# Kernel optimization log

Hardware: AMD Instinct MI355X
Metric: run time of the kernel (lower is better)

The kernel has to match this reference:

```python
import jax, jax.numpy as jnp
import numpy as np

B, S, D = 4, 2048, 512
E, K = 8, 2
MH = 4 * D      # resmlp mlp hidden
EH = 2 * D      # expert hidden
EPS = 1e-5


def setup_inputs() -> dict:
    key = jax.random.key(0)
    ks = jax.random.split(key, 16)
    s = 0.02
    return {
        "x": jax.random.normal(ks[0], (B, S, D), dtype=jnp.float32),
        "ln1_g": jnp.ones((D,), jnp.float32), "ln1_b": jnp.zeros((D,), jnp.float32),
        "w1": jax.random.normal(ks[1], (D, MH), jnp.float32) * s,
        "b1": jnp.zeros((MH,), jnp.float32),
        "w2": jax.random.normal(ks[2], (MH, D), jnp.float32) * s,
        "b2": jnp.zeros((D,), jnp.float32),
        "ln2_g": jnp.ones((D,), jnp.float32), "ln2_b": jnp.zeros((D,), jnp.float32),
        "wr": jax.random.normal(ks[3], (E, D), jnp.float32) * s,
        "ew1": jax.random.normal(ks[4], (E, D, EH), jnp.float32) * s,
        "eb1": jnp.zeros((E, EH), jnp.float32),
        "ew2": jax.random.normal(ks[5], (E, EH, D), jnp.float32) * s,
        "eb2": jnp.zeros((E, D), jnp.float32),
        "lnf_g": jnp.ones((D,), jnp.float32), "lnf_b": jnp.zeros((D,), jnp.float32),
    }


def _ln(z, g, b):
    m = z.mean(-1, keepdims=True)
    v = ((z - m) ** 2).mean(-1, keepdims=True)
    return (z - m) * jax.lax.rsqrt(v + EPS) * g + b


def reference(x, ln1_g, ln1_b, w1, b1, w2, b2, ln2_g, ln2_b,
              wr, ew1, eb1, ew2, eb2, lnf_g, lnf_b):
    # ---- ResidualMLPBlock (eval mode: dropout is identity) ----
    h = _ln(x, ln1_g, ln1_b)
    h = jax.nn.gelu(h @ w1 + b1, approximate=False) @ w2 + b2
    x = x + h
    x = _ln(x, ln2_g, ln2_b) + x
    # ---- MoE (eval: no jitter noise, aux_loss = 0) ----
    xf = x.reshape(-1, D)              # [N, D], N = B*S
    n = xf.shape[0]
    probs = jax.nn.softmax(xf @ wr.T, axis=-1)          # [N, E]
    topv, topi = jax.lax.top_k(probs, K)                # [N, K]
    topv = topv / topv.sum(-1, keepdims=True)
    # dense per-token gate per expert: sum over k of renormalized prob where idx==j
    gates = jnp.zeros((n, E), xf.dtype).at[jnp.arange(n)[:, None], topi].add(topv)
    # per-expert MLP over all tokens (masked scatter-combine via gates)
    he = jax.nn.gelu(jnp.einsum("nd,edh->enh", xf, ew1) + eb1[:, None, :],
                     approximate=False)                 # [E, N, 2D]
    ye = jnp.einsum("enh,ehd->end", he, ew2) + eb2[:, None, :]  # [E, N, D]
    out = jnp.einsum("ne,end->nd", gates, ye).reshape(B, S, D)
    # ---- final LayerNorm ----
    out = _ln(out, lnf_g, lnf_b)
    aux_loss = jnp.zeros((), x.dtype)  # eval mode
    return out, aux_loss
```

## Files before the change

### kernel.cpp

```cpp
#include <hip/hip_runtime.h>

#define NTOK 8192
#define DIM  512
#define MHID 2048
#define EHID 1024
#define NEXP 8
#define RBLK 64

using half_t = _Float16;
typedef _Float16 f16x8 __attribute__((ext_vector_type(8)));
typedef float    f32x16 __attribute__((ext_vector_type(16)));

#define MFMA32(a, b, c) __builtin_amdgcn_mfma_f32_32x32x16_f16((a), (b), (c), 0, 0, 0)

typedef const __attribute__((address_space(1))) void* gas_ptr;
typedef __attribute__((address_space(3))) void*       las_ptr;
__device__ __forceinline__ void gl16(const void* g, void* l) {
    __builtin_amdgcn_global_load_lds((gas_ptr)g, (las_ptr)l, 16, 0, 0);
}

__device__ __forceinline__ float gelu_exact(float v) {
    return 0.5f * v * (1.0f + erff(v * 0.70710678118654752f));
}

__device__ __forceinline__ float block_sum4(float v, float* red, int tid) {
#pragma unroll
    for (int off = 32; off; off >>= 1) v += __shfl_down(v, off);
    if ((tid & 63) == 0) red[tid >> 6] = v;
    __syncthreads();
    float r = red[0] + red[1] + red[2] + red[3];
    __syncthreads();
    return r;
}

__global__ __launch_bounds__(256) void ln1_split_kernel(
    const float* __restrict__ x, const float* __restrict__ g, const float* __restrict__ b,
    half_t* __restrict__ xh, half_t* __restrict__ xl)
{
    const int row = blockIdx.x, tid = threadIdx.x;
    __shared__ float red[4];
    const size_t base = (size_t)row * DIM;
    float2 v = reinterpret_cast<const float2*>(x + base)[tid];
    float mean = block_sum4(v.x + v.y, red, tid) * (1.0f / DIM);
    float d0 = v.x - mean, d1 = v.y - mean;
    float var = block_sum4(d0 * d0 + d1 * d1, red, tid) * (1.0f / DIM);
    float rstd = rsqrtf(var + 1e-5f);
    int d = tid * 2;
    float y0 = d0 * rstd * g[d]     + b[d];
    float y1 = d1 * rstd * g[d + 1] + b[d + 1];
    half_t h0 = (half_t)y0, h1 = (half_t)y1;
    xh[base + d] = h0;  xh[base + d + 1] = h1;
    xl[base + d]     = (half_t)(y0 - (float)h0);
    xl[base + d + 1] = (half_t)(y1 - (float)h1);
}

__global__ __launch_bounds__(256) void resid_ln2_kernel(
    const float* __restrict__ x, float* __restrict__ p0, const float* __restrict__ p1,
    const float* __restrict__ b2,
    const float* __restrict__ g, const float* __restrict__ b,
    half_t* __restrict__ x3h)
{
    const int row = blockIdx.x, tid = threadIdx.x;
    __shared__ float red[4];
    const size_t base = (size_t)row * DIM;
    float2 xv = reinterpret_cast<const float2*>(x + base)[tid];
    float2 h0 = reinterpret_cast<float2*>(p0 + base)[tid];
    float2 h1 = reinterpret_cast<const float2*>(p1 + base)[tid];
    float2 bb = reinterpret_cast<const float2*>(b2)[tid];
    float z0 = xv.x + h0.x + h1.x + bb.x, z1 = xv.y + h0.y + h1.y + bb.y;
    float mean = block_sum4(z0 + z1, red, tid) * (1.0f / DIM);
    float d0 = z0 - mean, d1 = z1 - mean;
    float var = block_sum4(d0 * d0 + d1 * d1, red, tid) * (1.0f / DIM);
    float rstd = rsqrtf(var + 1e-5f);
    int d = tid * 2;
    float y0 = d0 * rstd * g[d]     + b[d]     + z0;
    float y1 = d1 * rstd * g[d + 1] + b[d + 1] + z1;
    float2 o; o.x = y0; o.y = y1;
    reinterpret_cast<float2*>(p0 + base)[tid] = o;
    x3h[base + d]     = (half_t)y0;
    x3h[base + d + 1] = (half_t)y1;
}

__global__ void transpose_split_kernel(const float* __restrict__ in,
                                       half_t* __restrict__ oh, half_t* __restrict__ ol,
                                       int R, int C)
{
    __shared__ float t[32][33];
    const size_t mo = (size_t)blockIdx.z * (size_t)R * (size_t)C;
    const int c0 = blockIdx.x * 32, r0 = blockIdx.y * 32;
    const int tx = threadIdx.x, ty = threadIdx.y;
    for (int i = ty; i < 32; i += 8) t[i][tx] = in[mo + (size_t)(r0 + i) * C + c0 + tx];
    __syncthreads();
    for (int i = ty; i < 32; i += 8) {
        float v = t[tx][i];
        size_t o = mo + (size_t)(c0 + i) * R + r0 + tx;
        half_t h = (half_t)v;
        oh[o] = h;
        if (ol) ol[o] = (half_t)(v - (float)h);
    }
}

template <int EPI>
__global__ __launch_bounds__(256) void gemm3_kernel(
    const half_t* __restrict__ A0, const half_t* __restrict__ A1,
    const half_t* __restrict__ B0, const half_t* __restrict__ B1,
    const float* __restrict__ bias,
    float* __restrict__ Cf0, float* __restrict__ Cf1,
    half_t* __restrict__ Ch, half_t* __restrict__ Cl,
    int Nc, int K, int Ktile)
{
    __shared__ __align__(16) half_t As0[2][128 * 32];
    __shared__ __align__(16) half_t As1[2][128 * 32];
    __shared__ __align__(16) half_t Bs0[2][128 * 32];
    __shared__ __align__(16) half_t Bs1[2][128 * 32];
    const int m0 = blockIdx.x * 128, n0 = blockIdx.y * 128;
    const int kbeg = blockIdx.z * Ktile;
    float* Cf = blockIdx.z ? Cf1 : Cf0;
    const int tid = threadIdx.x;
    const int lane = tid & 63, wid = tid >> 6;
    const int wr = wid >> 1, wc = wid & 1;

    const int c0 = tid, c1 = tid + 256;
    const int r0 = c0 >> 2, s0 = (c0 & 3) ^ ((r0 >> 1) & 3);
    const int r1 = c1 >> 2, s1 = (c1 & 3) ^ ((r1 >> 1) & 3);
    const size_t aoff0 = (size_t)(m0 + r0) * K + kbeg + s0 * 8;
    const size_t aoff1 = (size_t)(m0 + r1) * K + kbeg + s1 * 8;
    const size_t boff0 = (size_t)(n0 + r0) * K + kbeg + s0 * 8;
    const size_t boff1 = (size_t)(n0 + r1) * K + kbeg + s1 * 8;

    const int l31 = lane & 31, l5 = lane >> 5;
    int oa[2][2], ob[2][2];
#pragma unroll
    for (int i = 0; i < 2; i++)
#pragma unroll
        for (int kh = 0; kh < 2; kh++) {
            int ra = wr * 64 + i * 32 + l31;
            oa[i][kh] = ra * 32 + (((l5 + kh * 2) ^ ((ra >> 1) & 3)) << 3);
            int rb = wc * 64 + i * 32 + l31;
            ob[i][kh] = rb * 32 + (((l5 + kh * 2) ^ ((rb >> 1) & 3)) << 3);
        }

    f32x16 acc[2][2];
#pragma unroll
    for (int i = 0; i < 2; i++)
#pragma unroll
        for (int j = 0; j < 2; j++)
#pragma unroll
            for (int q = 0; q < 16; q++) acc[i][j][q] = 0.f;

    auto stage = [&](int bsel, int k0) {
        gl16(A0 + aoff0 + k0, &As0[bsel][c0 * 8]);
        gl16(A0 + aoff1 + k0, &As0[bsel][c1 * 8]);
        gl16(A1 + aoff0 + k0, &As1[bsel][c0 * 8]);
        gl16(A1 + aoff1 + k0, &As1[bsel][c1 * 8]);
        gl16(B0 + boff0 + k0, &Bs0[bsel][c0 * 8]);
        gl16(B0 + boff1 + k0, &Bs0[bsel][c1 * 8]);
        gl16(B1 + boff0 + k0, &Bs1[bsel][c0 * 8]);
        gl16(B1 + boff1 + k0, &Bs1[bsel][c1 * 8]);
    };
    auto compute = [&](int bsel) {
#pragma unroll
        for (int kh = 0; kh < 2; kh++) {
            f16x8 ah0 = *(const f16x8*)(&As0[bsel][0] + oa[0][kh]);
            f16x8 ah1 = *(const f16x8*)(&As0[bsel][0] + oa[1][kh]);
            f16x8 al0 = *(const f16x8*)(&As1[bsel][0] + oa[0][kh]);
            f16x8 al1 = *(const f16x8*)(&As1[bsel][0] + oa[1][kh]);
            f16x8 bh0 = *(const f16x8*)(&Bs0[bsel][0] + ob[0][kh]);
            f16x8 bh1 = *(const f16x8*)(&Bs0[bsel][0] + ob[1][kh]);
            f16x8 bl0 = *(const f16x8*)(&Bs1[bsel][0] + ob[0][kh]);
            f16x8 bl1 = *(const f16x8*)(&Bs1[bsel][0] + ob[1][kh]);
            acc[0][0] = MFMA32(ah0, bh0, acc[0][0]);
            acc[0][0] = MFMA32(al0, bh0, acc[0][0]);
            acc[0][0] = MFMA32(ah0, bl0, acc[0][0]);
            acc[0][1] = MFMA32(ah0, bh1, acc[0][1]);
            acc[0][1] = MFMA32(al0, bh1, acc[0][1]);
            acc[0][1] = MFMA32(ah0, bl1, acc[0][1]);
            acc[1][0] = MFMA32(ah1, bh0, acc[1][0]);
            acc[1][0] = MFMA32(al1, bh0, acc[1][0]);
            acc[1][0] = MFMA32(ah1, bl0, acc[1][0]);
            acc[1][1] = MFMA32(ah1, bh1, acc[1][1]);
            acc[1][1] = MFMA32(al1, bh1, acc[1][1]);
            acc[1][1] = MFMA32(ah1, bl1, acc[1][1]);
        }
    };

    stage(0, 0);
#pragma unroll 1
    for (int k0 = 0; k0 < Ktile; k0 += 64) {
        __syncthreads();
        if (k0 + 32 < Ktile) stage(1, k0 + 32);
        compute(0);
        __syncthreads();
        if (k0 + 64 < Ktile) stage(0, k0 + 64);
        compute(1);
    }

    const int er = 4 * l5;
#pragma unroll
    for (int i = 0; i < 2; i++)
#pragma unroll
        for (int j = 0; j < 2; j++) {
            int cc = n0 + wc * 64 + j * 32 + l31;
            float bv = (EPI == 1) ? bias[cc] : 0.f;
#pragma unroll
            for (int reg = 0; reg < 16; reg++) {
                int rr = m0 + wr * 64 + i * 32 + er + 8 * (reg >> 2) + (reg & 3);
                float v = acc[i][j][reg] + bv;
                size_t o = (size_t)rr * Nc + cc;
                if (EPI == 1) {
                    float ge = gelu_exact(v);
                    half_t h = (half_t)ge;
                    Ch[o] = h;
                    Cl[o] = (half_t)(ge - (float)h);
                } else {
                    Cf[o] = v;
                }
            }
        }
}

__global__ __launch_bounds__(256) void router_kernel(
    const float* __restrict__ x3, const float* __restrict__ wrm,
    int* __restrict__ cnt, int* __restrict__ aid, float* __restrict__ gate)
{
    __shared__ float wl[NEXP][DIM];
    __shared__ int   texp[RBLK * 2];
    __shared__ float tgate[RBLK * 2];
    __shared__ int   lslot[RBLK * 2];
    __shared__ int   lcnt[NEXP], lbase[NEXP];
    const int tid = threadIdx.x;
    for (int i = tid; i < NEXP * DIM / 4; i += 256)
        reinterpret_cast<float4*>(&wl[0][0])[i] = reinterpret_cast<const float4*>(wrm)[i];
    if (tid < NEXP) lcnt[tid] = 0;
    __syncthreads();
    const int w = tid >> 6, lane = tid & 63;
#pragma unroll 1
    for (int t = 0; t < RBLK / 4; ++t) {
        const int lt = w * (RBLK / 4) + t;
        const int token = blockIdx.x * RBLK + lt;
        const float* xr = x3 + (size_t)token * DIM;
        float a[NEXP];
#pragma unroll
        for (int e = 0; e < NEXP; e++) a[e] = 0.f;
#pragma unroll
        for (int d0 = 0; d0 < DIM; d0 += 64) {
            float xv = xr[d0 + lane];
#pragma unroll
            for (int e = 0; e < NEXP; e++) a[e] += xv * wl[e][d0 + lane];
        }
#pragma unroll
        for (int e = 0; e < NEXP; e++)
#pragma unroll
            for (int off = 32; off; off >>= 1) a[e] += __shfl_xor(a[e], off);
        if (lane == 0) {
            int i1 = 0; float v1 = a[0];
#pragma unroll
            for (int e = 1; e < NEXP; e++) if (a[e] > v1) { v1 = a[e]; i1 = e; }
            int i2 = -1; float v2 = -3.4e38f;
#pragma unroll
            for (int e = 0; e < NEXP; e++) if (e != i1 && a[e] > v2) { v2 = a[e]; i2 = e; }
            float e2 = expf(v2 - v1);
            float g1 = 1.0f / (1.0f + e2);
            texp[lt * 2]      = i1; tgate[lt * 2]      = g1;
            texp[lt * 2 + 1]  = i2; tgate[lt * 2 + 1]  = 1.0f - g1;
        }
    }
    __syncthreads();
    if (tid < RBLK * 2) lslot[tid] = atomicAdd(&lcnt[texp[tid]], 1);
    __syncthreads();
    if (tid < NEXP) lbase[tid] = atomicAdd(&cnt[tid * 32], lcnt[tid]);
    __syncthreads();
    if (tid < RBLK * 2) {
        const int e = texp[tid];
        const int asg = blockIdx.x * (RBLK * 2) + tid;
        aid[e * NTOK + lbase[e] + lslot[tid]] = asg;
        gate[asg] = tgate[tid];
    }
}

__global__ __launch_bounds__(256) void egemm1_kernel(
    const half_t* __restrict__ X,
    const half_t* __restrict__ W,
    const float* __restrict__ eb1,
    const int* __restrict__ cnt, const int* __restrict__ aid,
    half_t* __restrict__ He)
{
    const int bid = blockIdx.x;
    const int e = bid >> 9, rem = bid & 511;
    const int mt = rem >> 3, nt = rem & 7;
    const int ne = cnt[e * 32];
    if (mt * 128 >= ne) return;
    __shared__ __align__(16) half_t As[2][128 * 32];
    __shared__ __align__(16) half_t Bs[2][128 * 32];
    __shared__ int rowmap[128];
    const int tid = threadIdx.x;
    if (tid < 128) {
        int slot = mt * 128 + tid;
        rowmap[tid] = (slot < ne) ? aid[e * NTOK + slot] : -1;
    }
    __syncthreads();
    const int lane = tid & 63, wid = tid >> 6;
    const int wr = wid >> 1, wc = wid & 1;
    const int c0 = tid, c1 = tid + 256;
    const int r0 = c0 >> 2, s0 = (c0 & 3) ^ ((r0 >> 1) & 3);
    const int r1 = c1 >> 2, s1 = (c1 & 3) ^ ((r1 >> 1) & 3);
    const int a0r = rowmap[r0], a1r = rowmap[r1];
    const half_t* pa0 = X + (size_t)(a0r >= 0 ? (a0r >> 1) : 0) * DIM + s0 * 8;
    const half_t* pa1 = X + (size_t)(a1r >= 0 ? (a1r >> 1) : 0) * DIM + s1 * 8;
    const half_t* pb0 = W + (size_t)e * EHID * DIM + (size_t)(nt * 128 + r0) * DIM + s0 * 8;
    const half_t* pb1 = W + (size_t)e * EHID * DIM + (size_t)(nt * 128 + r1) * DIM + s1 * 8;

    const int l31 = lane & 31, l5 = lane >> 5;
    int oa[2][2], ob[2][2];
#pragma unroll
    for (int i = 0; i < 2; i++)
#pragma unroll
        for (int kh = 0; kh < 2; kh++) {
            int ra = wr * 64 + i * 32 + l31;
            oa[i][kh] = ra * 32 + (((l5 + kh * 2) ^ ((ra >> 1) & 3)) << 3);
            int rb = wc * 64 + i * 32 + l31;
            ob[i][kh] = rb * 32 + (((l5 + kh * 2) ^ ((rb >> 1) & 3)) << 3);
        }
    f32x16 acc[2][2];
#pragma unroll
    for (int i = 0; i < 2; i++)
#pragma unroll
        for (int j = 0; j < 2; j++)
#pragma unroll
            for (int q = 0; q < 16; q++) acc[i][j][q] = 0.f;

    auto stage = [&](int bsel, int k0) {
        gl16(pa0 + k0, &As[bsel][c0 * 8]);
        gl16(pa1 + k0, &As[bsel][c1 * 8]);
        gl16(pb0 + k0, &Bs[bsel][c0 * 8]);
        gl16(pb1 + k0, &Bs[bsel][c1 * 8]);
    };
    auto compute = [&](int bsel) {
#pragma unroll
        for (int kh = 0; kh < 2; kh++) {
            f16x8 a0 = *(const f16x8*)(&As[bsel][0] + oa[0][kh]);
            f16x8 a1 = *(const f16x8*)(&As[bsel][0] + oa[1][kh]);
            f16x8 b0 = *(const f16x8*)(&Bs[bsel][0] + ob[0][kh]);
            f16x8 b1 = *(const f16x8*)(&Bs[bsel][0] + ob[1][kh]);
            acc[0][0] = MFMA32(a0, b0, acc[0][0]);
            acc[0][1] = MFMA32(a0, b1, acc[0][1]);
            acc[1][0] = MFMA32(a1, b0, acc[1][0]);
            acc[1][1] = MFMA32(a1, b1, acc[1][1]);
        }
    };

    stage(0, 0);
#pragma unroll 1
    for (int k0 = 0; k0 < DIM; k0 += 64) {
        __syncthreads();
        if (k0 + 32 < DIM) stage(1, k0 + 32);
        compute(0);
        __syncthreads();
        if (k0 + 64 < DIM) stage(0, k0 + 64);
        compute(1);
    }
    const int er = 4 * l5;
#pragma unroll
    for (int i = 0; i < 2; i++)
#pragma unroll
        for (int reg = 0; reg < 16; reg++) {
            int rloc = wr * 64 + i * 32 + er + 8 * (reg >> 2) + (reg & 3);
            int a = rowmap[rloc];
            if (a >= 0) {
#pragma unroll
                for (int j = 0; j < 2; j++) {
                    int cc = nt * 128 + wc * 64 + j * 32 + l31;
                    float v = acc[i][j][reg] + eb1[e * EHID + cc];
                    He[(size_t)a * EHID + cc] = (half_t)gelu_exact(v);
                }
            }
        }
}

__global__ __launch_bounds__(256) void egemm2_kernel(
    const half_t* __restrict__ Hin,
    const half_t* __restrict__ W,
    const float* __restrict__ eb2,
    const int* __restrict__ cnt, const int* __restrict__ aid,
    const float* __restrict__ gate,
    float* __restrict__ Ye)
{
    const int bid = blockIdx.x;
    const int e = bid >> 8, rem = bid & 255;
    const int mt = rem >> 2, nt = rem & 3;
    const int ne = cnt[e * 32];
    if (mt * 128 >= ne) return;
    __shared__ __align__(16) half_t As[2][128 * 32];
    __shared__ __align__(16) half_t Bs[2][128 * 32];
    __shared__ int rowmap[128];
    const int tid = threadIdx.x;
    if (tid < 128) {
        int slot = mt * 128 + tid;
        rowmap[tid] = (slot < ne) ? aid[e * NTOK + slot] : -1;
    }
    __syncthreads();
    const int lane = tid & 63, wid = tid >> 6;
    const int wr = wid >> 1, wc = wid & 1;
    const int c0 = tid, c1 = tid + 256;
    const int r0 = c0 >> 2, s0 = (c0 & 3) ^ ((r0 >> 1) & 3);
    const int r1 = c1 >> 2, s1 = (c1 & 3) ^ ((r1 >> 1) & 3);
    const int a0r = rowmap[r0], a1r = rowmap[r1];
    const half_t* pa0 = Hin + (size_t)(a0r >= 0 ? a0r : 0) * EHID + s0 * 8;
    const half_t* pa1 = Hin + (size_t)(a1r >= 0 ? a1r : 0) * EHID + s1 * 8;
    const half_t* pb0 = W + (size_t)e * DIM * EHID + (size_t)(nt * 128 + r0) * EHID + s0 * 8;
    const half_t* pb1 = W + (size_t)e * DIM * EHID + (size_t)(nt * 128 + r1) * EHID + s1 * 8;

    const int l31 = lane & 31, l5 = lane >> 5;
    int oa[2][2], ob[2][2];
#pragma unroll
    for (int i = 0; i < 2; i++)
#pragma unroll
        for (int kh = 0; kh < 2; kh++) {
            int ra = wr * 64 + i * 32 + l31;
            oa[i][kh] = ra * 32 + (((l5 + kh * 2) ^ ((ra >> 1) & 3)) << 3);
            int rb = wc * 64 + i * 32 + l31;
            ob[i][kh] = rb * 32 + (((l5 + kh * 2) ^ ((rb >> 1) & 3)) << 3);
        }
    f32x16 acc[2][2];
#pragma unroll
    for (int i = 0; i < 2; i++)
#pragma unroll
        for (int j = 0; j < 2; j++)
#pragma unroll
            for (int q = 0; q < 16; q++) acc[i][j][q] = 0.f;

    auto stage = [&](int bsel, int k0) {
        gl16(pa0 + k0, &As[bsel][c0 * 8]);
        gl16(pa1 + k0, &As[bsel][c1 * 8]);
        gl16(pb0 + k0, &Bs[bsel][c0 * 8]);
        gl16(pb1 + k0, &Bs[bsel][c1 * 8]);
    };
    auto compute = [&](int bsel) {
#pragma unroll
        for (int kh = 0; kh < 2; kh++) {
            f16x8 a0 = *(const f16x8*)(&As[bsel][0] + oa[0][kh]);
            f16x8 a1 = *(const f16x8*)(&As[bsel][0] + oa[1][kh]);
            f16x8 b0 = *(const f16x8*)(&Bs[bsel][0] + ob[0][kh]);
            f16x8 b1 = *(const f16x8*)(&Bs[bsel][0] + ob[1][kh]);
            acc[0][0] = MFMA32(a0, b0, acc[0][0]);
            acc[0][1] = MFMA32(a0, b1, acc[0][1]);
            acc[1][0] = MFMA32(a1, b0, acc[1][0]);
            acc[1][1] = MFMA32(a1, b1, acc[1][1]);
        }
    };

    stage(0, 0);
#pragma unroll 1
    for (int k0 = 0; k0 < EHID; k0 += 64) {
        __syncthreads();
        if (k0 + 32 < EHID) stage(1, k0 + 32);
        compute(0);
        __syncthreads();
        if (k0 + 64 < EHID) stage(0, k0 + 64);
        compute(1);
    }
    const int er = 4 * l5;
#pragma unroll
    for (int i = 0; i < 2; i++)
#pragma unroll
        for (int reg = 0; reg < 16; reg++) {
            int rloc = wr * 64 + i * 32 + er + 8 * (reg >> 2) + (reg & 3);
            int a = rowmap[rloc];
            if (a >= 0) {
                float gv = gate[a];
#pragma unroll
                for (int j = 0; j < 2; j++) {
                    int cc = nt * 128 + wc * 64 + j * 32 + l31;
                    float v = (acc[i][j][reg] + eb2[e * DIM + cc]) * gv;
                    Ye[(size_t)a * DIM + cc] = v;
                }
            }
        }
}

__global__ __launch_bounds__(256) void combine_lnf_kernel(
    const float* __restrict__ Ye, const float* __restrict__ g, const float* __restrict__ b,
    float* __restrict__ out)
{
    const int t = blockIdx.x, tid = threadIdx.x;
    __shared__ float red[4];
    float2 y0 = reinterpret_cast<const float2*>(Ye + (size_t)(2 * t) * DIM)[tid];
    float2 y1 = reinterpret_cast<const float2*>(Ye + (size_t)(2 * t + 1) * DIM)[tid];
    float z0 = y0.x + y1.x, z1 = y0.y + y1.y;
    float mean = block_sum4(z0 + z1, red, tid) * (1.0f / DIM);
    float d0 = z0 - mean, d1 = z1 - mean;
    float var = block_sum4(d0 * d0 + d1 * d1, red, tid) * (1.0f / DIM);
    float rstd = rsqrtf(var + 1e-5f);
    int d = tid * 2;
    out[(size_t)t * DIM + d]     = d0 * rstd * g[d]     + b[d];
    out[(size_t)t * DIM + d + 1] = d1 * rstd * g[d + 1] + b[d + 1];
    if (t == 0 && tid == 0) out[(size_t)NTOK * DIM] = 0.f;
}

__global__ void zero_cnt_kernel(int* cnt) {
    cnt[threadIdx.x] = 0;
}

extern "C" void kernel_launch(void* const* d_in, const int* in_sizes, int n_in,
                              void* d_out, int out_size, void* d_ws, size_t ws_size,
                              hipStream_t stream)
{
    (void)in_sizes; (void)n_in; (void)out_size; (void)ws_size;
    const float* x    = (const float*)d_in[0];
    const float* ln1g = (const float*)d_in[1];
    const float* ln1b = (const float*)d_in[2];
    const float* w1   = (const float*)d_in[3];
    const float* b1   = (const float*)d_in[4];
    const float* w2   = (const float*)d_in[5];
    const float* b2   = (const float*)d_in[6];
    const float* ln2g = (const float*)d_in[7];
    const float* ln2b = (const float*)d_in[8];
    const float* wrm  = (const float*)d_in[9];
    const float* ew1  = (const float*)d_in[10];
    const float* eb1  = (const float*)d_in[11];
    const float* ew2  = (const float*)d_in[12];
    const float* eb2  = (const float*)d_in[13];
    const float* lnfg = (const float*)d_in[14];
    const float* lnfb = (const float*)d_in[15];
    float* out = (float*)d_out;

    char* w = (char*)d_ws;
    size_t off = 0;
    auto take = [&](size_t bytes) {
        char* p = w + off;
        off += bytes;
        off = (off + 255) & ~(size_t)255;
        return p;
    };
    half_t* xh_h  = (half_t*)take((size_t)NTOK * DIM * 2);
    half_t* xh_l  = (half_t*)take((size_t)NTOK * DIM * 2);
    half_t* w1t_h = (half_t*)take((size_t)DIM * MHID * 2);
    half_t* w1t_l = (half_t*)take((size_t)DIM * MHID * 2);
    half_t* w2t_h = (half_t*)take((size_t)MHID * DIM * 2);
    half_t* w2t_l = (half_t*)take((size_t)MHID * DIM * 2);
    char*   big   = take((size_t)NTOK * MHID * 2 * 2);
    half_t* a1h   = (half_t*)big;
    half_t* a1l   = (half_t*)(big + (size_t)NTOK * MHID * 2);
    half_t* heh   = (half_t*)big;
    float*  yef   = (float*)(big + (size_t)NTOK * MHID * 2);
    float*  x3f   = (float*)take((size_t)NTOK * DIM * 4);
    half_t* x3h   = (half_t*)take((size_t)NTOK * DIM * 2);
    half_t* ew1t  = (half_t*)take((size_t)NEXP * DIM * EHID * 2);
    half_t* ew2t  = (half_t*)take((size_t)NEXP * EHID * DIM * 2);
    int*    cnt   = (int*)take(1024);
    int*    aid   = (int*)take((size_t)NEXP * NTOK * 4);
    float*  gate  = (float*)take((size_t)NTOK * 2 * 4);

    float* p0 = x3f;
    float* p1 = (float*)xh_h;

    zero_cnt_kernel<<<1, 256, 0, stream>>>(cnt);
    ln1_split_kernel<<<NTOK, 256, 0, stream>>>(x, ln1g, ln1b, xh_h, xh_l);
    transpose_split_kernel<<<dim3(MHID / 32, DIM / 32, 1), dim3(32, 8), 0, stream>>>(w1, w1t_h, w1t_l, DIM, MHID);
    transpose_split_kernel<<<dim3(DIM / 32, MHID / 32, 1), dim3(32, 8), 0, stream>>>(w2, w2t_h, w2t_l, MHID, DIM);
    transpose_split_kernel<<<dim3(EHID / 32, DIM / 32, NEXP), dim3(32, 8), 0, stream>>>(ew1, ew1t, (half_t*)0, DIM, EHID);
    transpose_split_kernel<<<dim3(DIM / 32, EHID / 32, NEXP), dim3(32, 8), 0, stream>>>(ew2, ew2t, (half_t*)0, EHID, DIM);
    gemm3_kernel<1><<<dim3(NTOK / 128, MHID / 128, 1), 256, 0, stream>>>(
        xh_h, xh_l, w1t_h, w1t_l, b1, (float*)0, (float*)0, a1h, a1l, MHID, DIM, DIM);
    gemm3_kernel<0><<<dim3(NTOK / 128, DIM / 128, 2), 256, 0, stream>>>(
        a1h, a1l, w2t_h, w2t_l, (const float*)0, p0, p1, (half_t*)0, (half_t*)0, DIM, MHID, MHID / 2);
    resid_ln2_kernel<<<NTOK, 256, 0, stream>>>(x, p0, p1, b2, ln2g, ln2b, x3h);
    router_kernel<<<NTOK / RBLK, 256, 0, stream>>>(x3f, wrm, cnt, aid, gate);
    egemm1_kernel<<<NEXP * (NTOK / 128) * (EHID / 128), 256, 0, stream>>>(x3h, ew1t, eb1, cnt, aid, heh);
    egemm2_kernel<<<NEXP * (NTOK / 128) * (DIM / 128), 256, 0, stream>>>(heh, ew2t, eb2, cnt, aid, gate, yef);
    combine_lnf_kernel<<<NTOK, 256, 0, stream>>>(yef, lnfg, lnfb, out);
}
```

Before: 326.9 us.

## Enlarge residual-MLP split-precision GEMM tiles to 256-row, 8-wave blocks

Replaces the 128x128, 4-wave split-fp16 GEMM with a 512-thread kernel using 256x256 (first GEMM) or 256x128 (second GEMM) tiles. Each wave holds a 4xNREP grid of 32x32 accumulators, which raises operand reuse per LDS load. The pipeline now uses explicit vmcnt waits and raw s_barrier with one LDS buffer per k-step, and raises wave priority with s_setprio around the MFMA bursts. In exchange it uses more registers and LDS per block and launches fewer blocks, which may lower occupancy and load balance across CUs.

```diff
diff --git a/kernel.cpp b/kernel.cpp
--- a/kernel.cpp
+++ b/kernel.cpp
@@ -100,8 +100,8 @@
     }
 }
 
-template <int EPI>
-__global__ __launch_bounds__(256) void gemm3_kernel(
+template <int EPI, int NREP>
+__global__ __launch_bounds__(512, 2) void gemm8_kernel(
     const half_t* __restrict__ A0, const half_t* __restrict__ A1,
     const half_t* __restrict__ B0, const half_t* __restrict__ B1,
     const float* __restrict__ bias,
@@ -109,103 +109,122 @@
     half_t* __restrict__ Ch, half_t* __restrict__ Cl,
     int Nc, int K, int Ktile)
 {
-    __shared__ __align__(16) half_t As0[2][128 * 32];
-    __shared__ __align__(16) half_t As1[2][128 * 32];
-    __shared__ __align__(16) half_t Bs0[2][128 * 32];
-    __shared__ __align__(16) half_t Bs1[2][128 * 32];
-    const int m0 = blockIdx.x * 128, n0 = blockIdx.y * 128;
+    constexpr int BN    = NREP * 128;
+    constexpr int LOADS = 4 + 2 * NREP;
+    constexpr int TOT   = 16384 + NREP * 8192;
+    __shared__ __align__(16) half_t lds[2 * TOT];
+
+    const int m0 = blockIdx.x * 256, n0 = blockIdx.y * BN;
     const int kbeg = blockIdx.z * Ktile;
     float* Cf = blockIdx.z ? Cf1 : Cf0;
     const int tid = threadIdx.x;
     const int lane = tid & 63, wid = tid >> 6;
-    const int wr = wid >> 1, wc = wid & 1;
-
-    const int c0 = tid, c1 = tid + 256;
-    const int r0 = c0 >> 2, s0 = (c0 & 3) ^ ((r0 >> 1) & 3);
-    const int r1 = c1 >> 2, s1 = (c1 & 3) ^ ((r1 >> 1) & 3);
-    const size_t aoff0 = (size_t)(m0 + r0) * K + kbeg + s0 * 8;
-    const size_t aoff1 = (size_t)(m0 + r1) * K + kbeg + s1 * 8;
-    const size_t boff0 = (size_t)(n0 + r0) * K + kbeg + s0 * 8;
-    const size_t boff1 = (size_t)(n0 + r1) * K + kbeg + s1 * 8;
-
+    const int wr = wid >> 2, wc = wid & 3;
     const int l31 = lane & 31, l5 = lane >> 5;
-    int oa[2][2], ob[2][2];
-#pragma unroll
-    for (int i = 0; i < 2; i++)
+
+    const half_t* gsrc[LOADS];
+    {
+        const half_t* A0p = A0 + (size_t)m0 * K + kbeg;
+        const half_t* A1p = A1 + (size_t)m0 * K + kbeg;
+        const half_t* B0p = B0 + (size_t)n0 * K + kbeg;
+        const half_t* B1p = B1 + (size_t)n0 * K + kbeg;
+#pragma unroll
+        for (int i = 0; i < LOADS; i++) {
+            int c = tid + 512 * i;
+            const half_t* base; int cm;
+            if (c < 1024)                  { base = A0p; cm = c; }
+            else if (c < 2048)             { base = A1p; cm = c - 1024; }
+            else if (c < 2048 + NREP * 512){ base = B0p; cm = c - 2048; }
+            else                           { base = B1p; cm = c - 2048 - NREP * 512; }
+            int r = cm >> 2, ss = (cm & 3) ^ ((r >> 1) & 3);
+            gsrc[i] = base + (size_t)r * K + ss * 8;
+        }
+    }
+
+    int oa[4][2], ob[NREP][2];
+#pragma unroll
+    for (int m = 0; m < 4; m++)
 #pragma unroll
         for (int kh = 0; kh < 2; kh++) {
-            int ra = wr * 64 + i * 32 + l31;
-            oa[i][kh] = ra * 32 + (((l5 + kh * 2) ^ ((ra >> 1) & 3)) << 3);
-            int rb = wc * 64 + i * 32 + l31;
-            ob[i][kh] = rb * 32 + (((l5 + kh * 2) ^ ((rb >> 1) & 3)) << 3);
-        }
-
-    f32x16 acc[2][2];
-#pragma unroll
-    for (int i = 0; i < 2; i++)
-#pragma unroll
-        for (int j = 0; j < 2; j++)
-#pragma unroll
-            for (int q = 0; q < 16; q++) acc[i][j][q] = 0.f;
-
-    auto stage = [&](int bsel, int k0) {
-        gl16(A0 + aoff0 + k0, &As0[bsel][c0 * 8]);
-        gl16(A0 + aoff1 + k0, &As0[bsel][c1 * 8]);
-        gl16(A1 + aoff0 + k0, &As1[bsel][c0 * 8]);
-        gl16(A1 + aoff1 + k0, &As1[bsel][c1 * 8]);
-        gl16(B0 + boff0 + k0, &Bs0[bsel][c0 * 8]);
-        gl16(B0 + boff1 + k0, &Bs0[bsel][c1 * 8]);
-        gl16(B1 + boff0 + k0, &Bs1[bsel][c0 * 8]);
-        gl16(B1 + boff1 + k0, &Bs1[bsel][c1 * 8]);
-    };
-    auto compute = [&](int bsel) {
+            int ra = wr * 128 + m * 32 + l31;
+            oa[m][kh] = ra * 32 + (((l5 + 2 * kh) ^ ((ra >> 1) & 3)) << 3);
+        }
+#pragma unroll
+    for (int n = 0; n < NREP; n++)
 #pragma unroll
         for (int kh = 0; kh < 2; kh++) {
-            f16x8 ah0 = *(const f16x8*)(&As0[bsel][0] + oa[0][kh]);
-            f16x8 ah1 = *(const f16x8*)(&As0[bsel][0] + oa[1][kh]);
-            f16x8 al0 = *(const f16x8*)(&As1[bsel][0] + oa[0][kh]);
-            f16x8 al1 = *(const f16x8*)(&As1[bsel][0] + oa[1][kh]);
-            f16x8 bh0 = *(const f16x8*)(&Bs0[bsel][0] + ob[0][kh]);
-            f16x8 bh1 = *(const f16x8*)(&Bs0[bsel][0] + ob[1][kh]);
-            f16x8 bl0 = *(const f16x8*)(&Bs1[bsel][0] + ob[0][kh]);
-            f16x8 bl1 = *(const f16x8*)(&Bs1[bsel][0] + ob[1][kh]);
-            acc[0][0] = MFMA32(ah0, bh0, acc[0][0]);
-            acc[0][0] = MFMA32(al0, bh0, acc[0][0]);
-            acc[0][0] = MFMA32(ah0, bl0, acc[0][0]);
-            acc[0][1] = MFMA32(ah0, bh1, acc[0][1]);
-            acc[0][1] = MFMA32(al0, bh1, acc[0][1]);
-            acc[0][1] = MFMA32(ah0, bl1, acc[0][1]);
-            acc[1][0] = MFMA32(ah1, bh0, acc[1][0]);
-            acc[1][0] = MFMA32(al1, bh0, acc[1][0]);
-            acc[1][0] = MFMA32(ah1, bl0, acc[1][0]);
-            acc[1][1] = MFMA32(ah1, bh1, acc[1][1]);
-            acc[1][1] = MFMA32(al1, bh1, acc[1][1]);
-            acc[1][1] = MFMA32(ah1, bl1, acc[1][1]);
-        }
-    };
-
+            int rb = wc * (NREP * 32) + n * 32 + l31;
+            ob[n][kh] = rb * 32 + (((l5 + 2 * kh) ^ ((rb >> 1) & 3)) << 3);
+        }
+
+    f32x16 acc[4][NREP];
+#pragma unroll
+    for (int m = 0; m < 4; m++)
+#pragma unroll
+        for (int n = 0; n < NREP; n++)
+#pragma unroll
+            for (int q = 0; q < 16; q++) acc[m][n][q] = 0.f;
+
+    auto stage = [&](int bsel, int kof) {
+#pragma unroll
+        for (int i = 0; i < LOADS; i++)
+            gl16(gsrc[i] + kof, &lds[bsel * TOT + (tid + 512 * i) * 8]);
+    };
+    auto phase = [&](int p, int kh) {
+        const half_t* buf = &lds[p ? TOT : 0];
+        f16x8 ah[4], al[4], bh[NREP], bl[NREP];
+#pragma unroll
+        for (int m = 0; m < 4; m++) {
+            ah[m] = *(const f16x8*)(buf + oa[m][kh]);
+            al[m] = *(const f16x8*)(buf + 8192 + oa[m][kh]);
+        }
+#pragma unroll
+        for (int n = 0; n < NREP; n++) {
+            bh[n] = *(const f16x8*)(buf + 16384 + ob[n][kh]);
+            bl[n] = *(const f16x8*)(buf + 16384 + BN * 32 + ob[n][kh]);
+        }
+        __builtin_amdgcn_s_setprio(1);
+#pragma unroll
+        for (int m = 0; m < 4; m++)
+#pragma unroll
+            for (int n = 0; n < NREP; n++) {
+                acc[m][n] = MFMA32(ah[m], bh[n], acc[m][n]);
+                acc[m][n] = MFMA32(al[m], bh[n], acc[m][n]);
+                acc[m][n] = MFMA32(ah[m], bl[n], acc[m][n]);
+            }
+        __builtin_amdgcn_s_setprio(0);
+    };
+
+    const int nsteps = Ktile / 32;
     stage(0, 0);
 #pragma unroll 1
-    for (int k0 = 0; k0 < Ktile; k0 += 64) {
-        __syncthreads();
-        if (k0 + 32 < Ktile) stage(1, k0 + 32);
-        compute(0);
-        __syncthreads();
-        if (k0 + 64 < Ktile) stage(0, k0 + 64);
-        compute(1);
-    }
+    for (int s = 0; s < nsteps - 1; ++s) {
+        stage((s + 1) & 1, (s + 1) * 32);
+        if constexpr (NREP == 2) asm volatile("s_waitcnt vmcnt(8)" ::: "memory");
+        else                     asm volatile("s_waitcnt vmcnt(6)" ::: "memory");
+        __builtin_amdgcn_s_barrier();
+        phase(s & 1, 0);
+        __builtin_amdgcn_s_barrier();
+        phase(s & 1, 1);
+        __builtin_amdgcn_s_barrier();
+    }
+    asm volatile("s_waitcnt vmcnt(0)" ::: "memory");
+    __builtin_amdgcn_s_barrier();
+    phase((nsteps - 1) & 1, 0);
+    __builtin_amdgcn_s_barrier();
+    phase((nsteps - 1) & 1, 1);
 
     const int er = 4 * l5;
 #pragma unroll
-    for (int i = 0; i < 2; i++)
-#pragma unroll
-        for (int j = 0; j < 2; j++) {
-            int cc = n0 + wc * 64 + j * 32 + l31;
+    for (int m = 0; m < 4; m++)
+#pragma unroll
+        for (int n = 0; n < NREP; n++) {
+            int cc = n0 + wc * (NREP * 32) + n * 32 + l31;
             float bv = (EPI == 1) ? bias[cc] : 0.f;
 #pragma unroll
             for (int reg = 0; reg < 16; reg++) {
-                int rr = m0 + wr * 64 + i * 32 + er + 8 * (reg >> 2) + (reg & 3);
-                float v = acc[i][j][reg] + bv;
+                int rr = m0 + wr * 128 + m * 32 + er + 8 * (reg >> 2) + (reg & 3);
+                float v = acc[m][n][reg] + bv;
                 size_t o = (size_t)rr * Nc + cc;
                 if (EPI == 1) {
                     float ge = gelu_exact(v);
@@ -560,9 +579,9 @@
     transpose_split_kernel<<<dim3(DIM / 32, MHID / 32, 1), dim3(32, 8), 0, stream>>>(w2, w2t_h, w2t_l, MHID, DIM);
     transpose_split_kernel<<<dim3(EHID / 32, DIM / 32, NEXP), dim3(32, 8), 0, stream>>>(ew1, ew1t, (half_t*)0, DIM, EHID);
     transpose_split_kernel<<<dim3(DIM / 32, EHID / 32, NEXP), dim3(32, 8), 0, stream>>>(ew2, ew2t, (half_t*)0, EHID, DIM);
-    gemm3_kernel<1><<<dim3(NTOK / 128, MHID / 128, 1), 256, 0, stream>>>(
+    gemm8_kernel<1, 2><<<dim3(NTOK / 256, MHID / 256, 1), 512, 0, stream>>>(
         xh_h, xh_l, w1t_h, w1t_l, b1, (float*)0, (float*)0, a1h, a1l, MHID, DIM, DIM);
-    gemm3_kernel<0><<<dim3(NTOK / 128, DIM / 128, 2), 256, 0, stream>>>(
+    gemm8_kernel<0, 1><<<dim3(NTOK / 256, DIM / 128, 2), 512, 0, stream>>>(
         a1h, a1l, w2t_h, w2t_l, (const float*)0, p0, p1, (half_t*)0, (half_t*)0, DIM, MHID, MHID / 2);
     resid_ln2_kernel<<<NTOK, 256, 0, stream>>>(x, p0, p1, b2, ln2g, ln2b, x3h);
     router_kernel<<<NTOK / RBLK, 256, 0, stream>>>(x3f, wrm, cnt, aid, gate);
```

Result: faster. 320.2 us (-2.1%).
